# Optimization experiments

Measured on AMD Instinct MI355X. Metric: run time of the kernel, lower is better.

Reference implementation:

```python
import jax, jax.numpy as jnp
import numpy as np

E = 128            # emb_size
N_TEXT = 40000     # text entities
N_NONTEXT = 10000  # non-text entities
N = N_TEXT + N_NONTEXT
N_EDGES = 300000
N_REL = 500
I = 3              # num_intents
ROUNDS = 2
RROUNDS = 2
PE = 2             # topic one-hot width
PRED_IN = 5 * E + 2 * PE + 2 * PE * (ROUNDS + RROUNDS)  # 5*128+4+16 = 660


def setup_inputs() -> dict:
    key = jax.random.key(0)
    ks = jax.random.split(key, 12)
    return {
        "h_id_tensor": jax.random.randint(ks[0], (N_EDGES,), 0, N, dtype=jnp.int64 if jax.config.jax_enable_x64 else jnp.int32).astype(jnp.int32),
        "r_id_tensor": jax.random.randint(ks[1], (N_EDGES,), 0, N_REL).astype(jnp.int32),
        "t_id_tensor": jax.random.randint(ks[2], (N_EDGES,), 0, N).astype(jnp.int32),
        "q_emb": jax.random.normal(ks[3], (1, E), dtype=jnp.float32),
        "entity_embs": jax.random.normal(ks[4], (N_TEXT, E), dtype=jnp.float32),
        "num_non_text_entities": N_NONTEXT,
        "relation_embs": jax.random.normal(ks[5], (N_REL, E), dtype=jnp.float32),
        "topic_entity_one_hot": jax.random.uniform(ks[6], (N, PE), dtype=jnp.float32),
        # learned params
        "non_text_entity_emb": jax.random.normal(ks[7], (1, E), dtype=jnp.float32),
        "intent_embs": jax.random.normal(ks[8], (I, E), dtype=jnp.float32),
        "W1": jax.random.normal(ks[9], (PRED_IN, E), dtype=jnp.float32) * 0.02,
        "b1": jnp.zeros((E,), dtype=jnp.float32),
        "W2": jax.random.normal(ks[10], (E, 1), dtype=jnp.float32) * 0.02,
        "b2": jnp.zeros((1,), dtype=jnp.float32),
    }


def _peconv(x, src, dst, n, inv_cnt):
    # mean aggregation: gather x at src, scatter-mean into dst
    s = jax.ops.segment_sum(x[src], dst, num_segments=n)
    return s * inv_cnt


def reference(h_id_tensor, r_id_tensor, t_id_tensor, q_emb, entity_embs,
              num_non_text_entities, relation_embs, topic_entity_one_hot,
              non_text_entity_emb, intent_embs, W1, b1, W2, b2):
    n = topic_entity_one_hot.shape[0]
    h_e0 = jnp.concatenate(
        [entity_embs, jnp.broadcast_to(non_text_entity_emb, (num_non_text_entities, E))], axis=0)  # [N,E]

    ones = jnp.ones((h_id_tensor.shape[0], 1), jnp.float32)
    cnt_fwd = jax.ops.segment_sum(ones, t_id_tensor, num_segments=n)  # in-degree via (h->t)
    cnt_rev = jax.ops.segment_sum(ones, h_id_tensor, num_segments=n)
    inv_fwd = 1.0 / jnp.maximum(cnt_fwd, 1.0)
    inv_rev = 1.0 / jnp.maximum(cnt_rev, 1.0)

    h_e_list = [h_e0, topic_entity_one_hot]
    h_pe = topic_entity_one_hot
    for _ in range(ROUNDS):
        h_pe = _peconv(h_pe, h_id_tensor, t_id_tensor, n, inv_fwd)
        h_e_list.append(h_pe)
    h_pe = topic_entity_one_hot
    for _ in range(RROUNDS):
        h_pe = _peconv(h_pe, t_id_tensor, h_id_tensor, n, inv_rev)
        h_e_list.append(h_pe)
    h_e = jnp.concatenate(h_e_list, axis=1)  # [N, E + 2 + 2*4]

    h_r = relation_embs[r_id_tensor]         # [T, E]
    h_head = h_e[h_id_tensor]                # [T, E+10]
    h_tail = h_e[t_id_tensor]                # [T, E+10]
    T = h_r.shape[0]
    h_q = jnp.broadcast_to(q_emb, (T, E))

    logits = []
    for i in range(intent_embs.shape[0]):
        iv = jnp.broadcast_to(intent_embs[i][None, :], (T, E))
        h_triple = jnp.concatenate([iv, h_q, h_head, h_r, h_tail], axis=1)  # [T, PRED_IN]
        h = jnp.maximum(h_triple @ W1 + b1, 0.0)
        logits.append(h @ W2 + b2)
    return jnp.concatenate(logits, axis=1)  # [T, I]
```

## Files before the change

### kernel.cpp

```cpp
#include <hip/hip_runtime.h>

#define E 128
#define OFF_Q 128
#define OFF_HEAD 256
#define OFF_REL 394
#define OFF_TAIL 522
#define KTOT 138
#define KP 160
#define AST 168
#define RNGC 2048
#define NCHK 8
#define CAP 16384

typedef __attribute__((ext_vector_type(8))) short short8;
typedef __attribute__((ext_vector_type(4))) float f32x4;

__device__ __forceinline__ unsigned short f2bf(float f) {
    unsigned u = __float_as_uint(f);
    return (unsigned short)((u + 0x7fffu + ((u >> 16) & 1u)) >> 16);
}
__device__ __forceinline__ unsigned bpack(float lo, float hi) {
    return (unsigned)f2bf(lo) | ((unsigned)f2bf(hi) << 16);
}
__device__ __forceinline__ float blo(unsigned u) { return __uint_as_float(u << 16); }
__device__ __forceinline__ float bhi(unsigned u) { return __uint_as_float(u & 0xffff0000u); }

__global__ __launch_bounds__(256) void bucket_prep_kernel(
        const int* __restrict__ h_id, const int* __restrict__ t_id,
        const float* __restrict__ rel, const float* __restrict__ intent,
        const float* __restrict__ q, const float* __restrict__ W1,
        const float* __restrict__ b1,
        unsigned* __restrict__ curs, unsigned* __restrict__ pairs_f,
        unsigned* __restrict__ pairs_r,
        unsigned short* __restrict__ rel_bf, float* __restrict__ bias3,
        unsigned short* __restrict__ W1T,
        int T, int bucketBlocks, int relBlocks, int biasBlocks, int NREL) {
    int tid = threadIdx.x;
    int bid = blockIdx.x;

    if (bid < bucketBlocks) {
        __shared__ unsigned hf[32], hr[32], basef[32], baser[32];
        if (tid < 32) { hf[tid] = 0; hr[tid] = 0; }
        __syncthreads();
        int e0 = (bid * 256 + tid) * 4;
        int hh[4], tt[4];
        int cnt = 0;
        if (e0 < T) {
            if (e0 + 3 < T) {
                int4 h4 = *(const int4*)&h_id[e0];
                int4 t4 = *(const int4*)&t_id[e0];
                hh[0] = h4.x; hh[1] = h4.y; hh[2] = h4.z; hh[3] = h4.w;
                tt[0] = t4.x; tt[1] = t4.y; tt[2] = t4.z; tt[3] = t4.w;
                cnt = 4;
            } else {
                for (int j = 0; e0 + j < T && j < 4; ++j) {
                    hh[j] = h_id[e0 + j];
                    tt[j] = t_id[e0 + j];
                    ++cnt;
                }
            }
        }
        unsigned bf[4], br[4];
        for (int j = 0; j < cnt; ++j) {
            bf[j] = (unsigned)tt[j] >> 11;
            br[j] = (unsigned)hh[j] >> 11;
            atomicAdd(&hf[bf[j]], 1u);
            atomicAdd(&hr[br[j]], 1u);
        }
        __syncthreads();
        if (tid < 32) {
            basef[tid] = hf[tid] ? atomicAdd(&curs[tid], hf[tid]) : 0u;
            baser[tid] = hr[tid] ? atomicAdd(&curs[32 + tid], hr[tid]) : 0u;
        }
        __syncthreads();
        if (tid < 32) { hf[tid] = 0; hr[tid] = 0; }
        __syncthreads();
        for (int j = 0; j < cnt; ++j) {
            unsigned sf = basef[bf[j]] + atomicAdd(&hf[bf[j]], 1u);
            if (sf < CAP) pairs_f[bf[j] * CAP + sf] =
                (unsigned)hh[j] | (((unsigned)tt[j] & 2047u) << 16);
            unsigned sr = baser[br[j]] + atomicAdd(&hr[br[j]], 1u);
            if (sr < CAP) pairs_r[br[j] * CAP + sr] =
                (unsigned)tt[j] | (((unsigned)hh[j] & 2047u) << 16);
        }
    } else if (bid < bucketBlocks + relBlocks) {
        int idx = (bid - bucketBlocks) * 256 + tid;
        int r = idx >> 7, j = idx & 127;
        if (r < NREL) {
            const float4* xr = (const float4*)(rel + (size_t)r * E);
            float acc = 0.f;
#pragma unroll
            for (int k4 = 0; k4 < 32; ++k4) {
                float4 x = xr[k4];
                int k = OFF_REL + k4 * 4;
                acc = fmaf(x.x, W1[(k + 0) * E + j], acc);
                acc = fmaf(x.y, W1[(k + 1) * E + j], acc);
                acc = fmaf(x.z, W1[(k + 2) * E + j], acc);
                acc = fmaf(x.w, W1[(k + 3) * E + j], acc);
            }
            rel_bf[idx] = f2bf(acc);
        }
    } else if (bid < bucketBlocks + relBlocks + biasBlocks) {
        int widx = (bid - bucketBlocks - relBlocks) * 4 + (tid >> 6);
        int lane = tid & 63;
        if (widx < 384) {
            int i = widx >> 7, j = widx & 127;
            float sum = 0.f;
#pragma unroll
            for (int m = 0; m < 4; ++m) {
                int k = lane + 64 * m;
                float x = (k < 128) ? intent[i * E + k] : q[k - 128];
                sum = fmaf(x, W1[(size_t)k * E + j], sum);
            }
#pragma unroll
            for (int o = 32; o > 0; o >>= 1) sum += __shfl_xor(sum, o, 64);
            if (lane == 0) bias3[i * E + j] = sum + b1[j];
        }
    } else {
        int c = bid - bucketBlocks - relBlocks - biasBlocks;
        if (tid < KP) {
            int cc = (c < 128) ? c : c - 128;
            int base = (c < 128) ? OFF_HEAD : OFF_TAIL;
            float v = (tid < KTOT) ? W1[(size_t)(base + tid) * E + cc] : 0.f;
            W1T[(size_t)c * KP + tid] = f2bf(v);
        }
    }
}

__global__ __launch_bounds__(1024) void scat1_kernel(
        const unsigned* __restrict__ pairs_f, const unsigned* __restrict__ pairs_r,
        const unsigned* __restrict__ curs, const float* __restrict__ topic,
        float* __restrict__ part1) {
    __shared__ float bins[6][RNGC];
    int b = blockIdx.x;
    int ck = blockIdx.y;
    int tid = threadIdx.x;
    for (int i = tid; i < 6 * RNGC; i += 1024) ((float*)bins)[i] = 0.f;
    __syncthreads();
    unsigned cf = min(curs[b], (unsigned)CAP);
    unsigned cr = min(curs[32 + b], (unsigned)CAP);
    const unsigned* pf = pairs_f + (size_t)b * CAP;
    const unsigned* pr = pairs_r + (size_t)b * CAP;
    unsigned lf = (cf + NCHK - 1) / NCHK;
    unsigned lr = (cr + NCHK - 1) / NCHK;
    unsigned f0 = ck * lf, f1e = min(cf, f0 + lf);
    unsigned r0 = ck * lr, r1e = min(cr, r0 + lr);
    for (unsigned i = f0 + tid; i < f1e; i += 1024) {
        unsigned p = pf[i];
        float2 v = *(const float2*)&topic[2 * (size_t)(p & 0xFFFFu)];
        int dl = p >> 16;
        atomicAdd(&bins[0][dl], v.x);
        atomicAdd(&bins[1][dl], v.y);
        atomicAdd(&bins[2][dl], 1.0f);
    }
    for (unsigned i = r0 + tid; i < r1e; i += 1024) {
        unsigned p = pr[i];
        float2 v = *(const float2*)&topic[2 * (size_t)(p & 0xFFFFu)];
        int dl = p >> 16;
        atomicAdd(&bins[3][dl], v.x);
        atomicAdd(&bins[4][dl], v.y);
        atomicAdd(&bins[5][dl], 1.0f);
    }
    __syncthreads();
    float* dst = part1 + ((size_t)(b * NCHK + ck) * 6) * RNGC;
#pragma unroll
    for (int c = 0; c < 6; ++c)
        for (int n = tid; n < RNGC; n += 1024)
            dst[c * RNGC + n] = bins[c][n];
}

__global__ __launch_bounds__(256) void reduce1_kernel(
        const float* __restrict__ part1,
        float* __restrict__ pef1, float* __restrict__ per1,
        float* __restrict__ inv_fwd, float* __restrict__ inv_rev, int N) {
    int n = blockIdx.x * 256 + threadIdx.x;
    if (n >= N) return;
    int b = n >> 11, nl = n & 2047;
    float s[6] = {0.f, 0.f, 0.f, 0.f, 0.f, 0.f};
    const float* base = part1 + (size_t)b * NCHK * 6 * RNGC + nl;
#pragma unroll
    for (int ck = 0; ck < NCHK; ++ck)
#pragma unroll
        for (int c = 0; c < 6; ++c)
            s[c] += base[(ck * 6 + c) * RNGC];
    float invf = 1.0f / fmaxf(s[2], 1.0f);
    float invr = 1.0f / fmaxf(s[5], 1.0f);
    pef1[2 * n] = s[0] * invf;
    pef1[2 * n + 1] = s[1] * invf;
    per1[2 * n] = s[3] * invr;
    per1[2 * n + 1] = s[4] * invr;
    inv_fwd[n] = invf;
    inv_rev[n] = invr;
}

__global__ __launch_bounds__(1024) void scat2_kernel(
        const unsigned* __restrict__ pairs_f, const unsigned* __restrict__ pairs_r,
        const unsigned* __restrict__ curs,
        const float* __restrict__ pef1, const float* __restrict__ per1,
        float* __restrict__ part2) {
    __shared__ float bins[4][RNGC];
    int b = blockIdx.x;
    int ck = blockIdx.y;
    int tid = threadIdx.x;
    for (int i = tid; i < 4 * RNGC; i += 1024) ((float*)bins)[i] = 0.f;
    __syncthreads();
    unsigned cf = min(curs[b], (unsigned)CAP);
    unsigned cr = min(curs[32 + b], (unsigned)CAP);
    const unsigned* pf = pairs_f + (size_t)b * CAP;
    const unsigned* pr = pairs_r + (size_t)b * CAP;
    unsigned lf = (cf + NCHK - 1) / NCHK;
    unsigned lr = (cr + NCHK - 1) / NCHK;
    unsigned f0 = ck * lf, f1e = min(cf, f0 + lf);
    unsigned r0 = ck * lr, r1e = min(cr, r0 + lr);
    for (unsigned i = f0 + tid; i < f1e; i += 1024) {
        unsigned p = pf[i];
        float2 v = *(const float2*)&pef1[2 * (size_t)(p & 0xFFFFu)];
        int dl = p >> 16;
        atomicAdd(&bins[0][dl], v.x);
        atomicAdd(&bins[1][dl], v.y);
    }
    for (unsigned i = r0 + tid; i < r1e; i += 1024) {
        unsigned p = pr[i];
        float2 v = *(const float2*)&per1[2 * (size_t)(p & 0xFFFFu)];
        int dl = p >> 16;
        atomicAdd(&bins[2][dl], v.x);
        atomicAdd(&bins[3][dl], v.y);
    }
    __syncthreads();
    float* dst = part2 + ((size_t)(b * NCHK + ck) * 4) * RNGC;
#pragma unroll
    for (int c = 0; c < 4; ++c)
        for (int n = tid; n < RNGC; n += 1024)
            dst[c * RNGC + n] = bins[c][n];
}

__global__ __launch_bounds__(256) void nodepre_mfma(
        const float* __restrict__ ent, const float* __restrict__ nontext,
        const float* __restrict__ topic,
        const float* __restrict__ pef1, const float* __restrict__ per1,
        const float* __restrict__ part2,
        const float* __restrict__ inv_fwd, const float* __restrict__ inv_rev,
        const unsigned short* __restrict__ W1T,
        unsigned short* __restrict__ head_bf, unsigned short* __restrict__ tail_bf,
        int N, int NTEXT) {
    __shared__ unsigned short As[64 * AST];
    int t = threadIdx.x;
    int lane = t & 63;
    int w = t >> 6;
    int l15 = lane & 15;
    int lg = lane >> 4;
    int n0 = blockIdx.x * 64;

    {
        int row = t >> 2, ch = t & 3;
        int node = n0 + row;
        bool ok = node < N;
        const float* src = (node < NTEXT) ? (ent + (size_t)node * E) : nontext;
        unsigned* dst = (unsigned*)&As[row * AST + ch * 32];
#pragma unroll
        for (int qq = 0; qq < 8; ++qq) {
            float4 v = ok ? *(const float4*)(src + ch * 32 + qq * 4)
                          : make_float4(0.f, 0.f, 0.f, 0.f);
            dst[qq * 2 + 0] = bpack(v.x, v.y);
            dst[qq * 2 + 1] = bpack(v.z, v.w);
        }
    }
    if (t < 64) {
        int node = n0 + t;
        bool ok = node < N;
        unsigned short* dst = &As[t * AST + 128];
        float ex[6];
        if (ok) {
            ex[0] = topic[2 * (size_t)node]; ex[1] = topic[2 * (size_t)node + 1];
            ex[2] = pef1[2 * (size_t)node];  ex[3] = pef1[2 * (size_t)node + 1];
            ex[4] = per1[2 * (size_t)node];  ex[5] = per1[2 * (size_t)node + 1];
        } else {
#pragma unroll
            for (int m = 0; m < 6; ++m) ex[m] = 0.f;
        }
        dst[0] = f2bf(ex[0]); dst[1] = f2bf(ex[1]);
        dst[2] = f2bf(ex[2]); dst[3] = f2bf(ex[3]);
        dst[6] = f2bf(ex[4]); dst[7] = f2bf(ex[5]);
#pragma unroll
        for (int m = 10; m < 32; ++m) dst[m] = 0;
    }
    {
        int nloc = t >> 2;
        int c = t & 3;
        int node = n0 + nloc;
        float val = 0.f;
        if (node < N) {
            int b = node >> 11, nl = node & 2047;
            const float* base = part2 + (size_t)b * NCHK * 4 * RNGC + nl;
            float s = 0.f;
#pragma unroll
            for (int ck = 0; ck < NCHK; ++ck)
                s += base[(ck * 4 + c) * RNGC];
            val = s * ((c < 2) ? inv_fwd[node] : inv_rev[node]);
        }
        int slot = (c < 2) ? (132 + c) : (134 + c);
        As[nloc * AST + (slot - 128) + 128] = f2bf(val);
    }
    __syncthreads();

    f32x4 zero = {0.f, 0.f, 0.f, 0.f};
    f32x4 acc[4][4];
#pragma unroll
    for (int rt = 0; rt < 4; ++rt)
#pragma unroll
        for (int ct = 0; ct < 4; ++ct) acc[rt][ct] = zero;

#pragma unroll
    for (int ks = 0; ks < 5; ++ks) {
        int kb = ks * 32 + lg * 8;
        short8 afrag[4];
#pragma unroll
        for (int rt = 0; rt < 4; ++rt)
            afrag[rt] = *(const short8*)&As[(rt * 16 + l15) * AST + kb];
#pragma unroll
        for (int ct = 0; ct < 4; ++ct) {
            int c = w * 64 + ct * 16 + l15;
            short8 b = *(const short8*)&W1T[(size_t)c * KP + kb];
#pragma unroll
            for (int rt = 0; rt < 4; ++rt)
                acc[rt][ct] = __builtin_amdgcn_mfma_f32_16x16x32_bf16(
                    afrag[rt], b, acc[rt][ct], 0, 0, 0);
        }
    }

#pragma unroll
    for (int rt = 0; rt < 4; ++rt) {
#pragma unroll
        for (int ct = 0; ct < 4; ++ct) {
            int c = w * 64 + ct * 16 + l15;
            unsigned short* base = (c < 128) ? head_bf : tail_bf;
            int cc = (c < 128) ? c : c - 128;
#pragma unroll
            for (int r = 0; r < 4; ++r) {
                int node = n0 + rt * 16 + lg * 4 + r;
                if (node < N) base[(size_t)node * E + cc] = f2bf(acc[rt][ct][r]);
            }
        }
    }
}

__global__ __launch_bounds__(256) void edge_kernel(
        const int* __restrict__ h_id, const int* __restrict__ r_id, const int* __restrict__ t_id,
        const unsigned short* __restrict__ head_bf, const unsigned short* __restrict__ rel_bf,
        const unsigned short* __restrict__ tail_bf, const float* __restrict__ bias3,
        const float* __restrict__ W2, const float* __restrict__ b2,
        float* __restrict__ out, int T) {
    int lane = threadIdx.x & 63;
    int sub = lane >> 4;
    int sl = lane & 15;
    int wid = blockIdx.x * (blockDim.x >> 6) + (threadIdx.x >> 6);
    int nw = gridDim.x * (blockDim.x >> 6);
    int c0 = sl * 8;

    float4 bi0a = *(const float4*)&bias3[c0],         bi0b = *(const float4*)&bias3[c0 + 4];
    float4 bi1a = *(const float4*)&bias3[E + c0],     bi1b = *(const float4*)&bias3[E + c0 + 4];
    float4 bi2a = *(const float4*)&bias3[2 * E + c0], bi2b = *(const float4*)&bias3[2 * E + c0 + 4];
    float4 w2a = *(const float4*)&W2[c0], w2b = *(const float4*)&W2[c0 + 4];
    float b2s = b2[0];

    int ne4 = (T + 3) >> 2;
    for (int e4 = wid; e4 < ne4; e4 += nw) {
        int e = e4 * 4 + sub;
        float p0 = 0.f, p1 = 0.f, p2 = 0.f;
        if (e < T) {
            int h = h_id[e], r = r_id[e], tt = t_id[e];
            uint4 hu = *(const uint4*)(head_bf + (size_t)h * E + c0);
            uint4 ru = *(const uint4*)(rel_bf + (size_t)r * E + c0);
            uint4 tu = *(const uint4*)(tail_bf + (size_t)tt * E + c0);
            float s[8];
            s[0] = blo(hu.x) + blo(ru.x) + blo(tu.x);
            s[1] = bhi(hu.x) + bhi(ru.x) + bhi(tu.x);
            s[2] = blo(hu.y) + blo(ru.y) + blo(tu.y);
            s[3] = bhi(hu.y) + bhi(ru.y) + bhi(tu.y);
            s[4] = blo(hu.z) + blo(ru.z) + blo(tu.z);
            s[5] = bhi(hu.z) + bhi(ru.z) + bhi(tu.z);
            s[6] = blo(hu.w) + blo(ru.w) + blo(tu.w);
            s[7] = bhi(hu.w) + bhi(ru.w) + bhi(tu.w);
            float bi0[8] = {bi0a.x, bi0a.y, bi0a.z, bi0a.w, bi0b.x, bi0b.y, bi0b.z, bi0b.w};
            float bi1[8] = {bi1a.x, bi1a.y, bi1a.z, bi1a.w, bi1b.x, bi1b.y, bi1b.z, bi1b.w};
            float bi2[8] = {bi2a.x, bi2a.y, bi2a.z, bi2a.w, bi2b.x, bi2b.y, bi2b.z, bi2b.w};
            float w2v[8] = {w2a.x, w2a.y, w2a.z, w2a.w, w2b.x, w2b.y, w2b.z, w2b.w};
#pragma unroll
            for (int j = 0; j < 8; ++j) {
                p0 = fmaf(fmaxf(s[j] + bi0[j], 0.f), w2v[j], p0);
                p1 = fmaf(fmaxf(s[j] + bi1[j], 0.f), w2v[j], p1);
                p2 = fmaf(fmaxf(s[j] + bi2[j], 0.f), w2v[j], p2);
            }
        }
#pragma unroll
        for (int o = 1; o < 16; o <<= 1) {
            p0 += __shfl_xor(p0, o, 64);
            p1 += __shfl_xor(p1, o, 64);
            p2 += __shfl_xor(p2, o, 64);
        }
        if (e < T && sl < 3) {
            float v = (sl == 0) ? p0 : ((sl == 1) ? p1 : p2);
            out[(size_t)e * 3 + sl] = v + b2s;
        }
    }
}

extern "C" void kernel_launch(void* const* d_in, const int* in_sizes, int n_in,
                              void* d_out, int out_size, void* d_ws, size_t ws_size,
                              hipStream_t stream) {
    const int* h_id = (const int*)d_in[0];
    const int* r_id = (const int*)d_in[1];
    const int* t_id = (const int*)d_in[2];
    const float* q = (const float*)d_in[3];
    const float* ent = (const float*)d_in[4];
    const float* rel = (const float*)d_in[6];
    const float* topic = (const float*)d_in[7];
    const float* nontext = (const float*)d_in[8];
    const float* intent = (const float*)d_in[9];
    const float* W1 = (const float*)d_in[10];
    const float* b1 = (const float*)d_in[11];
    const float* W2 = (const float*)d_in[12];
    const float* b2 = (const float*)d_in[13];

    int T = in_sizes[0];
    int NTEXT = in_sizes[4] / E;
    int N = in_sizes[7] / 2;
    int NREL = in_sizes[6] / E;

    int RC = (N + RNGC - 1) / RNGC;

    unsigned* curs = (unsigned*)d_ws;
    unsigned* pairs_f = curs + 64;
    unsigned* pairs_r = pairs_f + (size_t)32 * CAP;
    float* part1 = (float*)(pairs_r + (size_t)32 * CAP);
    float* inv_fwd = part1 + (size_t)RC * NCHK * 6 * RNGC;
    float* inv_rev = inv_fwd + N;
    float* pef1 = inv_rev + N;
    float* per1 = pef1 + 2 * (size_t)N;
    float* bias3 = per1 + 2 * (size_t)N;
    unsigned short* W1T = (unsigned short*)(bias3 + 3 * E);
    unsigned short* rel_bf = W1T + 256 * KP;
    unsigned short* head_bf = rel_bf + (size_t)NREL * E;
    unsigned short* tail_bf = head_bf + (size_t)N * E;

    const int tb = 256;
    int bucketBlocks = (T + tb * 4 - 1) / (tb * 4);
    int relBlocks = (NREL * E + tb - 1) / tb;
    int biasBlocks = 96;

    hipMemsetAsync(curs, 0, 64 * sizeof(unsigned), stream);

    bucket_prep_kernel<<<bucketBlocks + relBlocks + biasBlocks + 256, tb, 0, stream>>>(
        h_id, t_id, rel, intent, q, W1, b1, curs, pairs_f, pairs_r,
        rel_bf, bias3, W1T, T, bucketBlocks, relBlocks, biasBlocks, NREL);
    scat1_kernel<<<dim3(RC, NCHK), 1024, 0, stream>>>(pairs_f, pairs_r, curs, topic, part1);
    reduce1_kernel<<<(N + tb - 1) / tb, tb, 0, stream>>>(part1, pef1, per1, inv_fwd, inv_rev, N);
    scat2_kernel<<<dim3(RC, NCHK), 1024, 0, stream>>>(pairs_f, pairs_r, curs, pef1, per1, part1);
    nodepre_mfma<<<(N + 63) / 64, tb, 0, stream>>>(ent, nontext, topic, pef1, per1,
                                                   part1, inv_fwd, inv_rev, W1T,
                                                   head_bf, tail_bf, N, NTEXT);
    edge_kernel<<<2048, tb, 0, stream>>>(h_id, r_id, t_id, head_bf, rel_bf, tail_bf,
                                         bias3, W2, b2, (float*)d_out, T);
}
```

Baseline: 109.3 us.

## Process edges in tail-bucketed order to localize tail embedding gathers

The bucketing pass now also stores each edge's id and relation id alongside the forward (tail-bucketed) pairs. The final edge kernel walks these buckets, so each block's tail gathers fall in a 2048-node range that can stay in cache. Blocks are assigned so that neighbouring block ids map to different ranges. The cost is an extra workspace array and write in the prep kernel, scattered output writes, and a fixed 256-block grid whose chunks may be unbalanced.

```diff
diff --git a/kernel.cpp b/kernel.cpp
--- a/kernel.cpp
+++ b/kernel.cpp
@@ -26,12 +26,13 @@
 __device__ __forceinline__ float bhi(unsigned u) { return __uint_as_float(u & 0xffff0000u); }
 
 __global__ __launch_bounds__(256) void bucket_prep_kernel(
-        const int* __restrict__ h_id, const int* __restrict__ t_id,
+        const int* __restrict__ h_id, const int* __restrict__ r_id,
+        const int* __restrict__ t_id,
         const float* __restrict__ rel, const float* __restrict__ intent,
         const float* __restrict__ q, const float* __restrict__ W1,
         const float* __restrict__ b1,
         unsigned* __restrict__ curs, unsigned* __restrict__ pairs_f,
-        unsigned* __restrict__ pairs_r,
+        unsigned* __restrict__ eidr_f, unsigned* __restrict__ pairs_r,
         unsigned short* __restrict__ rel_bf, float* __restrict__ bias3,
         unsigned short* __restrict__ W1T,
         int T, int bucketBlocks, int relBlocks, int biasBlocks, int NREL) {
@@ -43,19 +44,22 @@
         if (tid < 32) { hf[tid] = 0; hr[tid] = 0; }
         __syncthreads();
         int e0 = (bid * 256 + tid) * 4;
-        int hh[4], tt[4];
+        int hh[4], tt[4], rr[4];
         int cnt = 0;
         if (e0 < T) {
             if (e0 + 3 < T) {
                 int4 h4 = *(const int4*)&h_id[e0];
                 int4 t4 = *(const int4*)&t_id[e0];
+                int4 r4 = *(const int4*)&r_id[e0];
                 hh[0] = h4.x; hh[1] = h4.y; hh[2] = h4.z; hh[3] = h4.w;
                 tt[0] = t4.x; tt[1] = t4.y; tt[2] = t4.z; tt[3] = t4.w;
+                rr[0] = r4.x; rr[1] = r4.y; rr[2] = r4.z; rr[3] = r4.w;
                 cnt = 4;
             } else {
                 for (int j = 0; e0 + j < T && j < 4; ++j) {
                     hh[j] = h_id[e0 + j];
                     tt[j] = t_id[e0 + j];
+                    rr[j] = r_id[e0 + j];
                     ++cnt;
                 }
             }
@@ -77,8 +81,12 @@
         __syncthreads();
         for (int j = 0; j < cnt; ++j) {
             unsigned sf = basef[bf[j]] + atomicAdd(&hf[bf[j]], 1u);
-            if (sf < CAP) pairs_f[bf[j] * CAP + sf] =
-                (unsigned)hh[j] | (((unsigned)tt[j] & 2047u) << 16);
+            if (sf < CAP) {
+                pairs_f[bf[j] * CAP + sf] =
+                    (unsigned)hh[j] | (((unsigned)tt[j] & 2047u) << 16);
+                eidr_f[bf[j] * CAP + sf] =
+                    (unsigned)(e0 + j) | ((unsigned)rr[j] << 19);
+            }
             unsigned sr = baser[br[j]] + atomicAdd(&hr[br[j]], 1u);
             if (sr < CAP) pairs_r[br[j] * CAP + sr] =
                 (unsigned)tt[j] | (((unsigned)hh[j] & 2047u) << 16);
@@ -344,17 +352,23 @@
     }
 }
 
-__global__ __launch_bounds__(256) void edge_kernel(
-        const int* __restrict__ h_id, const int* __restrict__ r_id, const int* __restrict__ t_id,
+__global__ __launch_bounds__(256) void edge2_kernel(
+        const unsigned* __restrict__ pairs_f, const unsigned* __restrict__ eidr_f,
+        const unsigned* __restrict__ curs,
         const unsigned short* __restrict__ head_bf, const unsigned short* __restrict__ rel_bf,
         const unsigned short* __restrict__ tail_bf, const float* __restrict__ bias3,
         const float* __restrict__ W2, const float* __restrict__ b2,
-        float* __restrict__ out, int T) {
+        float* __restrict__ out, int RC) {
+    int s = blockIdx.x & 7;
+    int idx = blockIdx.x >> 3;
+    int range = s + 8 * (idx >> 3);
+    int chunk = idx & 7;
+    if (range >= RC) return;
+
     int lane = threadIdx.x & 63;
     int sub = lane >> 4;
     int sl = lane & 15;
-    int wid = blockIdx.x * (blockDim.x >> 6) + (threadIdx.x >> 6);
-    int nw = gridDim.x * (blockDim.x >> 6);
+    int w = threadIdx.x >> 6;
     int c0 = sl * 8;
 
     float4 bi0a = *(const float4*)&bias3[c0],         bi0b = *(const float4*)&bias3[c0 + 4];
@@ -363,44 +377,57 @@
     float4 w2a = *(const float4*)&W2[c0], w2b = *(const float4*)&W2[c0 + 4];
     float b2s = b2[0];
 
-    int ne4 = (T + 3) >> 2;
-    for (int e4 = wid; e4 < ne4; e4 += nw) {
-        int e = e4 * 4 + sub;
+    unsigned cf = min(curs[range], (unsigned)CAP);
+    unsigned len = (cf + 7) >> 3;
+    unsigned i0 = chunk * len, i1 = min(cf, i0 + len);
+    const unsigned* pf = pairs_f + (size_t)range * CAP;
+    const unsigned* er = eidr_f + (size_t)range * CAP;
+    size_t tbase = (size_t)range * RNGC;
+
+    for (unsigned i = i0 + w * 4 + sub; ; i += 16) {
+        bool live = i < i1;
         float p0 = 0.f, p1 = 0.f, p2 = 0.f;
-        if (e < T) {
-            int h = h_id[e], r = r_id[e], tt = t_id[e];
+        unsigned eid = 0;
+        if (live) {
+            unsigned p = pf[i];
+            unsigned m = er[i];
+            unsigned h = p & 0xFFFFu;
+            unsigned tl = p >> 16;
+            unsigned r = m >> 19;
+            eid = m & 0x7FFFFu;
             uint4 hu = *(const uint4*)(head_bf + (size_t)h * E + c0);
             uint4 ru = *(const uint4*)(rel_bf + (size_t)r * E + c0);
-            uint4 tu = *(const uint4*)(tail_bf + (size_t)tt * E + c0);
-            float s[8];
-            s[0] = blo(hu.x) + blo(ru.x) + blo(tu.x);
-            s[1] = bhi(hu.x) + bhi(ru.x) + bhi(tu.x);
-            s[2] = blo(hu.y) + blo(ru.y) + blo(tu.y);
-            s[3] = bhi(hu.y) + bhi(ru.y) + bhi(tu.y);
-            s[4] = blo(hu.z) + blo(ru.z) + blo(tu.z);
-            s[5] = bhi(hu.z) + bhi(ru.z) + bhi(tu.z);
-            s[6] = blo(hu.w) + blo(ru.w) + blo(tu.w);
-            s[7] = bhi(hu.w) + bhi(ru.w) + bhi(tu.w);
+            uint4 tu = *(const uint4*)(tail_bf + (tbase + tl) * E + c0);
+            float sv[8];
+            sv[0] = blo(hu.x) + blo(ru.x) + blo(tu.x);
+            sv[1] = bhi(hu.x) + bhi(ru.x) + bhi(tu.x);
+            sv[2] = blo(hu.y) + blo(ru.y) + blo(tu.y);
+            sv[3] = bhi(hu.y) + bhi(ru.y) + bhi(tu.y);
+            sv[4] = blo(hu.z) + blo(ru.z) + blo(tu.z);
+            sv[5] = bhi(hu.z) + bhi(ru.z) + bhi(tu.z);
+            sv[6] = blo(hu.w) + blo(ru.w) + blo(tu.w);
+            sv[7] = bhi(hu.w) + bhi(ru.w) + bhi(tu.w);
             float bi0[8] = {bi0a.x, bi0a.y, bi0a.z, bi0a.w, bi0b.x, bi0b.y, bi0b.z, bi0b.w};
             float bi1[8] = {bi1a.x, bi1a.y, bi1a.z, bi1a.w, bi1b.x, bi1b.y, bi1b.z, bi1b.w};
             float bi2[8] = {bi2a.x, bi2a.y, bi2a.z, bi2a.w, bi2b.x, bi2b.y, bi2b.z, bi2b.w};
             float w2v[8] = {w2a.x, w2a.y, w2a.z, w2a.w, w2b.x, w2b.y, w2b.z, w2b.w};
 #pragma unroll
             for (int j = 0; j < 8; ++j) {
-                p0 = fmaf(fmaxf(s[j] + bi0[j], 0.f), w2v[j], p0);
-                p1 = fmaf(fmaxf(s[j] + bi1[j], 0.f), w2v[j], p1);
-                p2 = fmaf(fmaxf(s[j] + bi2[j], 0.f), w2v[j], p2);
-            }
-        }
+                p0 = fmaf(fmaxf(sv[j] + bi0[j], 0.f), w2v[j], p0);
+                p1 = fmaf(fmaxf(sv[j] + bi1[j], 0.f), w2v[j], p1);
+                p2 = fmaf(fmaxf(sv[j] + bi2[j], 0.f), w2v[j], p2);
+            }
+        }
+        if (__builtin_amdgcn_ballot_w64(live) == 0ull) break;
 #pragma unroll
         for (int o = 1; o < 16; o <<= 1) {
             p0 += __shfl_xor(p0, o, 64);
             p1 += __shfl_xor(p1, o, 64);
             p2 += __shfl_xor(p2, o, 64);
         }
-        if (e < T && sl < 3) {
+        if (live && sl < 3) {
             float v = (sl == 0) ? p0 : ((sl == 1) ? p1 : p2);
-            out[(size_t)e * 3 + sl] = v + b2s;
+            out[(size_t)eid * 3 + sl] = v + b2s;
         }
     }
 }
@@ -431,7 +458,8 @@
 
     unsigned* curs = (unsigned*)d_ws;
     unsigned* pairs_f = curs + 64;
-    unsigned* pairs_r = pairs_f + (size_t)32 * CAP;
+    unsigned* eidr_f = pairs_f + (size_t)32 * CAP;
+    unsigned* pairs_r = eidr_f + (size_t)32 * CAP;
     float* part1 = (float*)(pairs_r + (size_t)32 * CAP);
     float* inv_fwd = part1 + (size_t)RC * NCHK * 6 * RNGC;
     float* inv_rev = inv_fwd + N;
@@ -451,7 +479,7 @@
     hipMemsetAsync(curs, 0, 64 * sizeof(unsigned), stream);
 
     bucket_prep_kernel<<<bucketBlocks + relBlocks + biasBlocks + 256, tb, 0, stream>>>(
-        h_id, t_id, rel, intent, q, W1, b1, curs, pairs_f, pairs_r,
+        h_id, r_id, t_id, rel, intent, q, W1, b1, curs, pairs_f, eidr_f, pairs_r,
         rel_bf, bias3, W1T, T, bucketBlocks, relBlocks, biasBlocks, NREL);
     scat1_kernel<<<dim3(RC, NCHK), 1024, 0, stream>>>(pairs_f, pairs_r, curs, topic, part1);
     reduce1_kernel<<<(N + tb - 1) / tb, tb, 0, stream>>>(part1, pef1, per1, inv_fwd, inv_rev, N);
@@ -459,6 +487,6 @@
     nodepre_mfma<<<(N + 63) / 64, tb, 0, stream>>>(ent, nontext, topic, pef1, per1,
                                                    part1, inv_fwd, inv_rev, W1T,
                                                    head_bf, tail_bf, N, NTEXT);
-    edge_kernel<<<2048, tb, 0, stream>>>(h_id, r_id, t_id, head_bf, rel_bf, tail_bf,
-                                         bias3, W2, b2, (float*)d_out, T);
-}
+    edge2_kernel<<<256, tb, 0, stream>>>(pairs_f, eidr_f, curs, head_bf, rel_bf, tail_bf,
+                                         bias3, W2, b2, (float*)d_out, RC);
+}
```

Measured after the change: 187.4 us. 71.4% more time.
